# Optimization experiments

Hardware: AMD Instinct MI355X
Metric: run time of the kernel (lower is better)

## Reference

```python
import jax, jax.numpy as jnp
import numpy as np


def _conv(x, w):
    # SpykeTorch snn.Convolution: plain conv2d, no bias, no padding (VALID)
    return jax.lax.conv_general_dilated(
        x, w, window_strides=(1, 1), padding='VALID',
        dimension_numbers=('NCHW', 'OIHW', 'NCHW'))


def _pad2(x, p=2):
    # sf.pad(input, pad=(2,2,2,2), value=0): zero-pad last two (spatial) dims
    return jnp.pad(x, ((0, 0), (0, 0), (p, p), (p, p)))


def _fire(pot, thr):
    # sf.fire: thresholded[pot <= thr] = 0 ; spk = thresholded.sign()
    thresholded = jnp.where(pot > thr, pot, jnp.zeros((), pot.dtype))
    spk = (pot > thr).astype(pot.dtype)
    return spk, thresholded


def _pool(x, k, s):
    # sf.pooling: max_pool2d, floor mode (== VALID reduce_window)
    return jax.lax.reduce_window(
        x, -jnp.inf, jax.lax.max,
        window_dimensions=(1, 1, k, k),
        window_strides=(1, 1, s, s),
        padding='VALID')


def setup_inputs() -> dict:
    key = jax.random.key(0)
    kx, k1, k2, k3 = jax.random.split(key, 4)
    # (T, C, H, W): T timesteps act as batch in SpykeTorch
    x = jax.random.uniform(kx, (20, 6, 160, 160), dtype=jnp.float32)

    def xavier_normal(k, shape):
        fan_in = shape[1] * shape[2] * shape[3]
        fan_out = shape[0] * shape[2] * shape[3]
        std = float(np.sqrt(2.0 / (fan_in + fan_out)))
        return jax.random.normal(k, shape, dtype=jnp.float32) * std

    w1 = xavier_normal(k1, (30, 6, 4, 4))
    w2 = xavier_normal(k2, (250, 30, 3, 3))
    w3 = xavier_normal(k3, (200, 250, 3, 3))
    return {'x': x, 'w1': w1, 'w2': w2, 'w3': w3, 'layer_idx': 3}


def reference(x, w1, w2, w3, layer_idx):
    # Eval-mode forward path of deepSNN up to `layer_idx` (tensor-returning branches)
    CONV1_T, CONV2_T, CONV3_T = 1.0, 1.0, 25.0
    inp = _pad2(x.astype(jnp.float32))          # (T,6,164,164)
    pot = _conv(inp, w1)                        # (T,30,161,161)
    spk, pot = _fire(pot, CONV1_T)
    if layer_idx == 1:
        return spk, pot
    pot = _conv(_pad2(_pool(spk, 2, 2)), w2)    # (T,250,82,82)
    spk, pot = _fire(pot, CONV2_T)
    if layer_idx == 2:
        return spk, pot
    pot = _conv(_pad2(_pool(spk, 3, 3)), w3)    # (T,200,29,29)
    spk, pot = _fire(pot, CONV3_T)
    return spk, pot
```

## Files before the change

kernel.cpp:

```cpp
#include <hip/hip_runtime.h>
#include <hip/hip_bf16.h>
#include <hip/hip_fp16.h>


#define OUT_HALF 3364000
#define MASK_PLANE 128000
#define T_FLOATS 168200

typedef float f32x16 __attribute__((ext_vector_type(16)));
typedef short bf8s __attribute__((ext_vector_type(8)));
typedef float f32x4 __attribute__((ext_vector_type(4)));
typedef float v2f __attribute__((ext_vector_type(2)));
typedef f32x4 f32x4u __attribute__((aligned(4)));

static __device__ __forceinline__ unsigned int pkbf(float a, float b) {
    union { __hip_bfloat162 h; unsigned int u; } cv;
    cv.h = __float22bfloat162_rn(make_float2(a, b));
    return cv.u;
}
static __device__ __forceinline__ unsigned short bfbits(float a) {
    union { __hip_bfloat16 h; unsigned short u; } cv;
    cv.h = __float2bfloat16(a);
    return cv.u;
}
static __device__ __forceinline__ v2f up2(unsigned int u) {
    union { unsigned int u32; __half2 h2; } cv; cv.u32 = u;
    float2 f = __half22float2(cv.h2);
    v2f r; r.x = f.x; r.y = f.y;
    return r;
}
static __device__ __forceinline__ unsigned long long expand32(unsigned int v) {
    unsigned long long x = v;
    x = (x | (x << 16)) & 0x0000FFFF0000FFFFull;
    x = (x | (x << 8))  & 0x00FF00FF00FF00FFull;
    x = (x | (x << 4))  & 0x0F0F0F0F0F0F0F0Full;
    x = (x | (x << 2))  & 0x3333333333333333ull;
    x = (x | (x << 1))  & 0x5555555555555555ull;
    return x;
}

__global__ __launch_bounds__(256) void k_conv1m(const float* __restrict__ x,
                                                const float* __restrict__ w1,
                                                const float* __restrict__ w2,
                                                unsigned int* __restrict__ w2h,
                                                unsigned int* __restrict__ mask1,
                                                unsigned int* __restrict__ flags2) {
    int tid = threadIdx.x;
    if (blockIdx.x >= 2000) {
        int tb = blockIdx.x - 2000;
        if (tb == 0)
            for (int i = tid; i < 540; i += 256) flags2[i] = 0u;
        int idx = tb * 256 + tid;
        int ck = idx >> 7, pl = idx & 127;
        int oc0 = 2 * pl, oc1 = oc0 + 1;
        float a = (oc0 < 250) ? w2[oc0 * 270 + ck] : 0.f;
        float bb = (oc1 < 250) ? w2[oc1 * 270 + ck] : 0.f;
        union { __half2 h2; unsigned int u; } cv;
        cv.h2.x = __float2half(a);
        cv.h2.y = __float2half(bb);
        w2h[idx] = cv.u;
        return;
    }

    __shared__ unsigned short B_lds[6 * 64 * 8];

#pragma unroll
    for (int n = 0; n < 12; ++n) {
        int q = n * 256 + tid;
        int i = q & 7, ll = (q >> 3) & 63, ks = q >> 9;
        int oc = ll & 31;
        int kg = ks * 16 + ((ll >> 5) << 3) + i;
        float w = (oc < 30) ? w1[oc * 96 + kg] : 0.f;
        B_lds[q] = bfbits(w);
    }
    __syncthreads();

    int l = tid & 63, wv = tid >> 6;
    int b = blockIdx.x;
    int t = b / 100;
    int u = (b % 100) * 4 + wv;
    int pr = u / 5, jblk = u % 5;
    int m = l & 31, hi = l >> 5;
    int j = jblk * 32 + m;

    bf8s bq[6];
#pragma unroll
    for (int ks = 0; ks < 6; ++ks)
        bq[ks] = *(const bf8s*)&B_lds[(ks * 64 + l) * 8];

    f32x16 acc0 = (f32x16)(0.0f);
    f32x16 acc1 = (f32x16)(0.0f);
    int sr0 = 2 * pr + 2 * hi - 2;
    int sc0 = j - 2;
    bool fast = ((unsigned)sr0 <= 157u) && ((unsigned)sc0 <= 156u);

#pragma unroll
    for (int ks = 0; ks < 6; ++ks) {
        const float* xp = x + (t * 6 + ks) * 25600;
        f32x4 v0, v1, v2;
        if (fast) {
            const float* bp = xp + sr0 * 160 + sc0;
            v0 = *(const f32x4u*)(bp);
            v1 = *(const f32x4u*)(bp + 160);
            v2 = *(const f32x4u*)(bp + 320);
        } else {
            float tmp[3][4];
#pragma unroll
            for (int r = 0; r < 3; ++r)
#pragma unroll
                for (int e = 0; e < 4; ++e) {
                    int sr = sr0 + r, sc = sc0 + e;
                    tmp[r][e] = ((unsigned)sr < 160u && (unsigned)sc < 160u)
                                    ? xp[sr * 160 + sc] : 0.f;
                }
            v0.x = tmp[0][0]; v0.y = tmp[0][1]; v0.z = tmp[0][2]; v0.w = tmp[0][3];
            v1.x = tmp[1][0]; v1.y = tmp[1][1]; v1.z = tmp[1][2]; v1.w = tmp[1][3];
            v2.x = tmp[2][0]; v2.y = tmp[2][1]; v2.z = tmp[2][2]; v2.w = tmp[2][3];
        }
        union { bf8s s; unsigned int u4[4]; } a0, a1;
        a0.u4[0] = pkbf(v0.x, v0.y);
        a0.u4[1] = pkbf(v0.z, v0.w);
        a0.u4[2] = pkbf(v1.x, v1.y);
        a0.u4[3] = pkbf(v1.z, v1.w);
        a1.u4[0] = a0.u4[2];
        a1.u4[1] = a0.u4[3];
        a1.u4[2] = pkbf(v2.x, v2.y);
        a1.u4[3] = pkbf(v2.z, v2.w);
        acc0 = __builtin_amdgcn_mfma_f32_32x32x16_bf16(a0.s, bq[ks], acc0, 0, 0, 0);
        acc1 = __builtin_amdgcn_mfma_f32_32x32x16_bf16(a1.s, bq[ks], acc1, 0, 0, 0);
    }

    unsigned int mbase = (unsigned int)((t * 80 + pr) * 80 + jblk * 16);
#pragma unroll
    for (int a = 0; a < 8; ++a) {
        bool s = acc0[2 * a] > 1.f || acc0[2 * a + 1] > 1.f ||
                 acc1[2 * a] > 1.f || acc1[2 * a + 1] > 1.f;
        unsigned long long bal = __ballot(s);
        if (l < 6) {
            int h = l >> 1;
            unsigned int word = (l & 1) ? (unsigned int)(bal >> 32)
                                        : (unsigned int)bal;
            int pc = (a & 1) + ((a >> 1) << 2) + ((l & 1) << 1);
            mask1[h * MASK_PLANE + mbase + pc] = (word >> (10 * h)) & 0x3FFu;
        }
    }
}

__global__ __launch_bounds__(256) void k_conv2(const unsigned int* __restrict__ mask1,
                                               const unsigned int* __restrict__ w2h,
                                               unsigned long long* __restrict__ pool2m,
                                               unsigned int* __restrict__ flags2) {
    __shared__ unsigned int m_lds[5 * 84];

    int b = blockIdx.x;
    int ninth = b % 9;  b /= 9;
    int ph = b % 27;
    int t = b / 27;
    int tid = threadIdx.x;
    int l = tid & 63, wv = tid >> 6;
    int h = wv & 1, grp = wv >> 1;
    int r0 = 3 * ph - 2;
    int pwA = ninth * 3;

    for (int idx = tid; idx < 420; idx += 256) {
        int r = idx / 84, col = idx % 84;
        int gr = r0 + r, gc = col - 2;
        unsigned int v = 0;
        if ((unsigned)gr < 80u && (unsigned)gc < 80u) {
            int i2 = (t * 80 + gr) * 80 + gc;
            v = mask1[i2] | (mask1[MASK_PLANE + i2] << 10) |
                (mask1[2 * MASK_PLANE + i2] << 20);
        }
        m_lds[idx] = v;
    }
    __syncthreads();

    const unsigned int* wb = w2h + h * 64 + l;
    unsigned long long* prow = pool2m + ((t * 27 + ph) * 27) * 4 + 2 * h;
    v2f z2 = (v2f)(0.f);

    if (grp == 0) {
        int c0A = 3 * pwA, c0B = c0A + 3;
        unsigned int qA[25], qB[25];
#pragma unroll
        for (int dr = 0; dr < 5; ++dr)
#pragma unroll
            for (int ds = 0; ds < 5; ++ds) {
                qA[dr * 5 + ds] = m_lds[dr * 84 + c0A + ds];
                qB[dr * 5 + ds] = m_lds[dr * 84 + c0B + ds];
            }

        v2f accA[3][3], accB[3][3];
#pragma unroll
        for (int i = 0; i < 3; ++i)
#pragma unroll
            for (int j = 0; j < 3; ++j) { accA[i][j] = z2; accB[i][j] = z2; }

#pragma unroll
        for (int dr = 0; dr < 5; ++dr) {
#pragma unroll
            for (int ds = 0; ds < 5; ++ds) {
                unsigned int mA = qA[dr * 5 + ds];
                unsigned int mB = qB[dr * 5 + ds];
                while (mA | mB) {
                    bool hA = mA != 0, hB = mB != 0;
                    int cA = __builtin_ctz(mA | 0x40000000u);
                    int cB = __builtin_ctz(mB | 0x40000000u);
                    mA &= mA - 1;
                    mB &= mB - 1;
                    const unsigned int* pA = wb + cA * 1152;
                    const unsigned int* pB = wb + cB * 1152;
                    unsigned int uA[3][3], uB[3][3];
#pragma unroll
                    for (int i = 0; i < 3; ++i) {
                        if (dr - i < 0 || dr - i > 2) continue;
#pragma unroll
                        for (int j = 0; j < 3; ++j) {
                            if (ds - j < 0 || ds - j > 2) continue;
                            int off = ((dr - i) * 3 + (ds - j)) * 128;
                            uA[i][j] = pA[off];
                            uB[i][j] = pB[off];
                        }
                    }
#pragma unroll
                    for (int i = 0; i < 3; ++i) {
                        if (dr - i < 0 || dr - i > 2) continue;
#pragma unroll
                        for (int j = 0; j < 3; ++j) {
                            if (ds - j < 0 || ds - j > 2) continue;
                            accA[i][j] += hA ? up2(uA[i][j]) : z2;
                            accB[i][j] += hB ? up2(uB[i][j]) : z2;
                        }
                    }
                }
            }
        }

        bool sA0 = false, sA1 = false, sB0 = false, sB1 = false;
#pragma unroll
        for (int i = 0; i < 3; ++i)
#pragma unroll
            for (int j = 0; j < 3; ++j) {
                sA0 = sA0 || (accA[i][j].x > 1.f);
                sA1 = sA1 || (accA[i][j].y > 1.f);
                sB0 = sB0 || (accB[i][j].x > 1.f);
                sB1 = sB1 || (accB[i][j].y > 1.f);
            }
        unsigned long long bA0 = __ballot(sA0), bA1 = __ballot(sA1);
        unsigned long long bB0 = __ballot(sB0), bB1 = __ballot(sB1);
        unsigned long long wA0 = expand32((unsigned int)bA0) |
                                 (expand32((unsigned int)bA1) << 1);
        unsigned long long wA1 = expand32((unsigned int)(bA0 >> 32)) |
                                 (expand32((unsigned int)(bA1 >> 32)) << 1);
        unsigned long long wB0 = expand32((unsigned int)bB0) |
                                 (expand32((unsigned int)bB1) << 1);
        unsigned long long wB1 = expand32((unsigned int)(bB0 >> 32)) |
                                 (expand32((unsigned int)(bB1 >> 32)) << 1);
        if (l == 0) {
            prow[pwA * 4]           = wA0;
            prow[pwA * 4 + 1]       = wA1;
            prow[(pwA + 1) * 4]     = wB0;
            prow[(pwA + 1) * 4 + 1] = wB1;
        }
        if ((wA0 | wA1 | wB0 | wB1) && l == 0)
            flags2[t * 27 + ph] = 1u;
    } else {
        int pw = pwA + 2;
        int c0 = 3 * pw;
        unsigned int q[25];
#pragma unroll
        for (int dr = 0; dr < 5; ++dr)
#pragma unroll
            for (int ds = 0; ds < 5; ++ds)
                q[dr * 5 + ds] = m_lds[dr * 84 + c0 + ds];

        v2f acc[3][3];
#pragma unroll
        for (int i = 0; i < 3; ++i)
#pragma unroll
            for (int j = 0; j < 3; ++j) acc[i][j] = z2;

#pragma unroll
        for (int dr = 0; dr < 5; ++dr) {
#pragma unroll
            for (int ds = 0; ds < 5; ++ds) {
                unsigned int m = q[dr * 5 + ds];
                while (m) {
                    int c1 = __builtin_ctz(m); m &= m - 1;
                    bool has2 = (m != 0);
                    int c2 = c1;
                    if (has2) { c2 = __builtin_ctz(m); m &= m - 1; }
                    const unsigned int* p1 = wb + c1 * 1152;
                    const unsigned int* p2 = wb + c2 * 1152;
                    unsigned int u1[3][3], u2[3][3];
#pragma unroll
                    for (int i = 0; i < 3; ++i) {
                        if (dr - i < 0 || dr - i > 2) continue;
#pragma unroll
                        for (int j = 0; j < 3; ++j) {
                            if (ds - j < 0 || ds - j > 2) continue;
                            int off = ((dr - i) * 3 + (ds - j)) * 128;
                            u1[i][j] = p1[off];
                            u2[i][j] = p2[off];
                        }
                    }
#pragma unroll
                    for (int i = 0; i < 3; ++i) {
                        if (dr - i < 0 || dr - i > 2) continue;
#pragma unroll
                        for (int j = 0; j < 3; ++j) {
                            if (ds - j < 0 || ds - j > 2) continue;
                            acc[i][j] += up2(u1[i][j]);
                            acc[i][j] += has2 ? up2(u2[i][j]) : z2;
                        }
                    }
                }
            }
        }

        bool s0 = false, s1 = false;
#pragma unroll
        for (int i = 0; i < 3; ++i)
#pragma unroll
            for (int j = 0; j < 3; ++j) {
                s0 = s0 || (acc[i][j].x > 1.f);
                s1 = s1 || (acc[i][j].y > 1.f);
            }
        unsigned long long b0 = __ballot(s0), b1 = __ballot(s1);
        unsigned long long w0 = expand32((unsigned int)b0) |
                                (expand32((unsigned int)b1) << 1);
        unsigned long long w1 = expand32((unsigned int)(b0 >> 32)) |
                                (expand32((unsigned int)(b1 >> 32)) << 1);
        if (l == 0) {
            prow[pw * 4]     = w0;
            prow[pw * 4 + 1] = w1;
        }
        if ((w0 | w1) && l == 0) flags2[t * 27 + ph] = 1u;
    }
}

__global__ __launch_bounds__(320) void k_conv3(const unsigned long long* __restrict__ pool2m,
                                               const float* __restrict__ w3,
                                               float* __restrict__ out,
                                               const unsigned int* __restrict__ flags2) {
    __shared__ float w_lds[25 * 9 * 40];
    __shared__ float in_lds[25 * 4 * 34];

    int b = blockIdx.x;
    int rb = b % 15;  b /= 15;
    int ocg = b % 5;  b /= 5;
    int t = b;
    int oc0 = ocg * 40;
    int r0 = 2 * rb;
    int tid = threadIdx.x;
    int ocl = tid % 40, ct = tid / 40;

    {
        unsigned int fT = 0;
        const unsigned int* fp = flags2 + t * 27;
#pragma unroll
        for (int r = 0; r < 27; ++r) fT |= fp[r];
        if (fT == 0) {
            float4 z; z.x = 0.f; z.y = 0.f; z.z = 0.f; z.w = 0.f;
            float4* o0 = (float4*)(out + (size_t)t * T_FLOATS);
            float4* o1 = (float4*)(out + OUT_HALF + (size_t)t * T_FLOATS);
            int s = ocg * 15 + rb;
            int lo = s * 561;
            int hi = lo + 561; if (hi > 42050) hi = 42050;
            for (int i = lo + tid; i < hi; i += 320) {
                o0[i] = z;
                o1[i] = z;
            }
            return;
        }
    }

    {
        unsigned int f = 0;
        int rlo = r0 - 2; if (rlo < 0) rlo = 0;
        int rhi = r0 + 1; if (rhi > 26) rhi = 26;
        for (int r = rlo; r <= rhi; ++r) f |= flags2[t * 27 + r];
        if (f == 0) {
            int nrows = (r0 + 1 < 29) ? 2 : 1;
            int stride = 29 * nrows;
            int cnt = 40 * stride;
            for (int idx = tid; idx < cnt; idx += 320) {
                int o = idx / stride, rem = idx % stride;
                size_t base = (size_t)((t * 200 + oc0 + o) * 29 + r0) * 29 + rem;
                out[base] = 0.f;
                out[OUT_HALF + base] = 0.f;
            }
            return;
        }
    }

    float acc[2][4];
#pragma unroll
    for (int i = 0; i < 2; ++i)
#pragma unroll
        for (int j = 0; j < 4; ++j) acc[i][j] = 0.f;

    for (int chn = 0; chn < 10; ++chn) {
        int cc0 = chn * 25;
        for (int idx = tid; idx < 25 * 9 * 40; idx += 320) {
            int o = idx % 40, ck = idx / 40;
            int ckg = cc0 * 9 + ck;
            w_lds[idx] = w3[(size_t)(oc0 + o) * 2250 + ckg];
        }
        for (int idx = tid; idx < 25 * 4 * 34; idx += 320) {
            int col = idx % 34;
            int rem = idx / 34;
            int r = rem & 3, cl = rem >> 2;
            int gr = r0 + r - 2, gc = col - 2;
            float v = 0.f;
            if ((unsigned)gr < 27u && (unsigned)gc < 27u) {
                int c = cc0 + cl;
                unsigned long long wbits =
                    pool2m[((t * 27 + gr) * 27 + gc) * 4 + (c >> 6)];
                v = (float)((wbits >> (c & 63)) & 1ull);
            }
            in_lds[idx] = v;
        }
        __syncthreads();

        for (int cl = 0; cl < 25; ++cl) {
            float in[4][6];
#pragma unroll
            for (int r = 0; r < 4; ++r)
#pragma unroll
                for (int j = 0; j < 6; ++j)
                    in[r][j] = in_lds[(cl * 4 + r) * 34 + ct * 4 + j];
            const float* wp = &w_lds[cl * 360 + ocl];
#pragma unroll
            for (int k = 0; k < 9; ++k) {
                float w = wp[k * 40];
                int kh = k / 3, kw = k % 3;
#pragma unroll
                for (int i = 0; i < 2; ++i)
#pragma unroll
                    for (int j = 0; j < 4; ++j)
                        acc[i][j] += in[i + kh][j + kw] * w;
            }
        }
        __syncthreads();
    }

    {
        int oc = oc0 + ocl;
#pragma unroll
        for (int i = 0; i < 2; ++i) {
            int r = r0 + i;
            if (r < 29) {
#pragma unroll
                for (int j = 0; j < 4; ++j) {
                    int col = ct * 4 + j;
                    if (col < 29) {
                        float pot = acc[i][j];
                        bool s = pot > 25.f;
                        size_t base = ((size_t)((t * 200 + oc) * 29 + r)) * 29 + col;
                        out[base] = s ? 1.f : 0.f;
                        out[OUT_HALF + base] = s ? pot : 0.f;
                    }
                }
            }
        }
    }
}

extern "C" void kernel_launch(void* const* d_in, const int* in_sizes, int n_in,
                              void* d_out, int out_size, void* d_ws, size_t ws_size,
                              hipStream_t stream) {
    const float* x  = (const float*)d_in[0];
    const float* w1 = (const float*)d_in[1];
    const float* w2 = (const float*)d_in[2];
    const float* w3 = (const float*)d_in[3];
    float* out = (float*)d_out;

    unsigned int* mask1 = (unsigned int*)d_ws;
    unsigned long long* pool2m = (unsigned long long*)((char*)d_ws + 1536000);
    unsigned int* w2h = (unsigned int*)((char*)d_ws + 2002560);
    unsigned int* flags2 = (unsigned int*)((char*)d_ws + 2277376);

    k_conv1m<<<2135, 256, 0, stream>>>(x, w1, w2, w2h, mask1, flags2);
    k_conv2<<<20 * 27 * 9, 256, 0, stream>>>(mask1, w2h, pool2m, flags2);
    k_conv3<<<20 * 5 * 15, 320, 0, stream>>>(pool2m, w3, out, flags2);
}
```

Baseline: 124.9 us.

## Replace sparse scalar conv2 with bf16 MFMA im2col over binary spike mask

Conv2 previously walked the set bits of the spike mask and accumulated fp16 weights in scalar registers. It now builds a dense bf16 im2col tile of 0/1 spikes in LDS and runs 32x32x16 bf16 MFMA with weights held in registers. The weight prepack changes to a bf16 fragment layout, and the grid becomes one 512-thread block per (t, pooled row) instead of nine per row. This removes divergent, data-dependent gather loops at the cost of doing dense work on sparse inputs, with bf16 rounding of the weights.

```diff
diff --git a/kernel.cpp b/kernel.cpp
--- a/kernel.cpp
+++ b/kernel.cpp
@@ -1,6 +1,5 @@
 #include <hip/hip_runtime.h>
 #include <hip/hip_bf16.h>
-#include <hip/hip_fp16.h>
 
 
 #define OUT_HALF 3364000
@@ -10,7 +9,6 @@
 typedef float f32x16 __attribute__((ext_vector_type(16)));
 typedef short bf8s __attribute__((ext_vector_type(8)));
 typedef float f32x4 __attribute__((ext_vector_type(4)));
-typedef float v2f __attribute__((ext_vector_type(2)));
 typedef f32x4 f32x4u __attribute__((aligned(4)));
 
 static __device__ __forceinline__ unsigned int pkbf(float a, float b) {
@@ -23,26 +21,11 @@
     cv.h = __float2bfloat16(a);
     return cv.u;
 }
-static __device__ __forceinline__ v2f up2(unsigned int u) {
-    union { unsigned int u32; __half2 h2; } cv; cv.u32 = u;
-    float2 f = __half22float2(cv.h2);
-    v2f r; r.x = f.x; r.y = f.y;
-    return r;
-}
-static __device__ __forceinline__ unsigned long long expand32(unsigned int v) {
-    unsigned long long x = v;
-    x = (x | (x << 16)) & 0x0000FFFF0000FFFFull;
-    x = (x | (x << 8))  & 0x00FF00FF00FF00FFull;
-    x = (x | (x << 4))  & 0x0F0F0F0F0F0F0F0Full;
-    x = (x | (x << 2))  & 0x3333333333333333ull;
-    x = (x | (x << 1))  & 0x5555555555555555ull;
-    return x;
-}
 
 __global__ __launch_bounds__(256) void k_conv1m(const float* __restrict__ x,
                                                 const float* __restrict__ w1,
                                                 const float* __restrict__ w2,
-                                                unsigned int* __restrict__ w2h,
+                                                unsigned short* __restrict__ w2b,
                                                 unsigned int* __restrict__ mask1,
                                                 unsigned int* __restrict__ flags2) {
     int tid = threadIdx.x;
@@ -51,14 +34,15 @@
         if (tb == 0)
             for (int i = tid; i < 540; i += 256) flags2[i] = 0u;
         int idx = tb * 256 + tid;
-        int ck = idx >> 7, pl = idx & 127;
-        int oc0 = 2 * pl, oc1 = oc0 + 1;
-        float a = (oc0 < 250) ? w2[oc0 * 270 + ck] : 0.f;
-        float bb = (oc1 < 250) ? w2[oc1 * 270 + ck] : 0.f;
-        union { __half2 h2; unsigned int u; } cv;
-        cv.h2.x = __float2half(a);
-        cv.h2.y = __float2half(bb);
-        w2h[idx] = cv.u;
+        int i8 = idx & 7;
+        int ll = (idx >> 3) & 63;
+        int gi = idx >> 9;
+        int ocg = (gi * 1928) >> 15;
+        int ks = gi - ocg * 17;
+        int oc = ocg * 32 + (ll & 31);
+        int k = ks * 16 + ((ll >> 5) << 3) + i8;
+        float w = (oc < 250 && k < 270) ? w2[oc * 270 + k] : 0.f;
+        w2b[idx] = bfbits(w);
         return;
     }
 
@@ -146,24 +130,30 @@
     }
 }
 
-__global__ __launch_bounds__(256) void k_conv2(const unsigned int* __restrict__ mask1,
-                                               const unsigned int* __restrict__ w2h,
-                                               unsigned long long* __restrict__ pool2m,
+__global__ __launch_bounds__(512) void k_conv2(const unsigned int* __restrict__ mask1,
+                                               const unsigned short* __restrict__ w2b,
+                                               unsigned int* __restrict__ pool2m32,
                                                unsigned int* __restrict__ flags2) {
     __shared__ unsigned int m_lds[5 * 84];
+    __shared__ unsigned short A_lds[96 * 280];
 
     int b = blockIdx.x;
-    int ninth = b % 9;  b /= 9;
-    int ph = b % 27;
-    int t = b / 27;
+    int ph = b % 27, t = b / 27;
     int tid = threadIdx.x;
     int l = tid & 63, wv = tid >> 6;
-    int h = wv & 1, grp = wv >> 1;
+    int m = l & 31, hi = l >> 5;
     int r0 = 3 * ph - 2;
-    int pwA = ninth * 3;
-
-    for (int idx = tid; idx < 420; idx += 256) {
-        int r = idx / 84, col = idx % 84;
+
+    bf8s bfr[17];
+    {
+        const unsigned short* wbp = w2b + (wv * 17 * 64 + l) * 8;
+#pragma unroll
+        for (int ks = 0; ks < 17; ++ks)
+            bfr[ks] = *(const bf8s*)(wbp + ks * 512);
+    }
+
+    if (tid < 420) {
+        int r = tid / 84, col = tid % 84;
         int gr = r0 + r, gc = col - 2;
         unsigned int v = 0;
         if ((unsigned)gr < 80u && (unsigned)gc < 80u) {
@@ -171,172 +161,91 @@
             v = mask1[i2] | (mask1[MASK_PLANE + i2] << 10) |
                 (mask1[2 * MASK_PLANE + i2] << 20);
         }
-        m_lds[idx] = v;
+        m_lds[tid] = v;
     }
     __syncthreads();
 
-    const unsigned int* wb = w2h + h * 64 + l;
-    unsigned long long* prow = pool2m + ((t * 27 + ph) * 27) * 4 + 2 * h;
-    v2f z2 = (v2f)(0.f);
-
-    if (grp == 0) {
-        int c0A = 3 * pwA, c0B = c0A + 3;
-        unsigned int qA[25], qB[25];
-#pragma unroll
-        for (int dr = 0; dr < 5; ++dr)
-#pragma unroll
-            for (int ds = 0; ds < 5; ++ds) {
-                qA[dr * 5 + ds] = m_lds[dr * 84 + c0A + ds];
-                qB[dr * 5 + ds] = m_lds[dr * 84 + c0B + ds];
-            }
-
-        v2f accA[3][3], accB[3][3];
-#pragma unroll
-        for (int i = 0; i < 3; ++i)
-#pragma unroll
-            for (int j = 0; j < 3; ++j) { accA[i][j] = z2; accB[i][j] = z2; }
-
-#pragma unroll
-        for (int dr = 0; dr < 5; ++dr) {
-#pragma unroll
-            for (int ds = 0; ds < 5; ++ds) {
-                unsigned int mA = qA[dr * 5 + ds];
-                unsigned int mB = qB[dr * 5 + ds];
-                while (mA | mB) {
-                    bool hA = mA != 0, hB = mB != 0;
-                    int cA = __builtin_ctz(mA | 0x40000000u);
-                    int cB = __builtin_ctz(mB | 0x40000000u);
-                    mA &= mA - 1;
-                    mB &= mB - 1;
-                    const unsigned int* pA = wb + cA * 1152;
-                    const unsigned int* pB = wb + cB * 1152;
-                    unsigned int uA[3][3], uB[3][3];
-#pragma unroll
-                    for (int i = 0; i < 3; ++i) {
-                        if (dr - i < 0 || dr - i > 2) continue;
-#pragma unroll
-                        for (int j = 0; j < 3; ++j) {
-                            if (ds - j < 0 || ds - j > 2) continue;
-                            int off = ((dr - i) * 3 + (ds - j)) * 128;
-                            uA[i][j] = pA[off];
-                            uB[i][j] = pB[off];
-                        }
-                    }
-#pragma unroll
-                    for (int i = 0; i < 3; ++i) {
-                        if (dr - i < 0 || dr - i > 2) continue;
-#pragma unroll
-                        for (int j = 0; j < 3; ++j) {
-                            if (ds - j < 0 || ds - j > 2) continue;
-                            accA[i][j] += hA ? up2(uA[i][j]) : z2;
-                            accB[i][j] += hB ? up2(uB[i][j]) : z2;
-                        }
-                    }
+    unsigned int rowor[3] = {0u, 0u, 0u};
+
+#pragma unroll
+    for (int rho = 0; rho < 3; ++rho) {
+        if (rho > 0) __syncthreads();
+
+        if (tid < 164) {
+            int s = tid >> 1;
+            unsigned int w[9];
+#pragma unroll
+            for (int tp = 0; tp < 9; ++tp)
+                w[tp] = m_lds[(rho + tp / 3) * 84 + s + (tp % 3)];
+            if ((tid & 1) == 0) {
+                unsigned int* dst = (unsigned int*)&A_lds[s * 280];
+#pragma unroll
+                for (int kp = 0; kp < 68; ++kp) {
+                    const int k0 = 2 * kp, k1 = k0 + 1;
+                    unsigned int v = 0;
+                    { const int c = k0 / 9, tp = k0 % 9;
+                      v |= ((w[tp] >> c) & 1u) ? 0x3F80u : 0u; }
+                    { const int c = k1 / 9, tp = k1 % 9;
+                      v |= ((w[tp] >> c) & 1u) ? 0x3F800000u : 0u; }
+                    dst[kp] = v;
                 }
-            }
-        }
-
-        bool sA0 = false, sA1 = false, sB0 = false, sB1 = false;
-#pragma unroll
-        for (int i = 0; i < 3; ++i)
-#pragma unroll
-            for (int j = 0; j < 3; ++j) {
-                sA0 = sA0 || (accA[i][j].x > 1.f);
-                sA1 = sA1 || (accA[i][j].y > 1.f);
-                sB0 = sB0 || (accB[i][j].x > 1.f);
-                sB1 = sB1 || (accB[i][j].y > 1.f);
-            }
-        unsigned long long bA0 = __ballot(sA0), bA1 = __ballot(sA1);
-        unsigned long long bB0 = __ballot(sB0), bB1 = __ballot(sB1);
-        unsigned long long wA0 = expand32((unsigned int)bA0) |
-                                 (expand32((unsigned int)bA1) << 1);
-        unsigned long long wA1 = expand32((unsigned int)(bA0 >> 32)) |
-                                 (expand32((unsigned int)(bA1 >> 32)) << 1);
-        unsigned long long wB0 = expand32((unsigned int)bB0) |
-                                 (expand32((unsigned int)bB1) << 1);
-        unsigned long long wB1 = expand32((unsigned int)(bB0 >> 32)) |
-                                 (expand32((unsigned int)(bB1 >> 32)) << 1);
-        if (l == 0) {
-            prow[pwA * 4]           = wA0;
-            prow[pwA * 4 + 1]       = wA1;
-            prow[(pwA + 1) * 4]     = wB0;
-            prow[(pwA + 1) * 4 + 1] = wB1;
-        }
-        if ((wA0 | wA1 | wB0 | wB1) && l == 0)
-            flags2[t * 27 + ph] = 1u;
-    } else {
-        int pw = pwA + 2;
-        int c0 = 3 * pw;
-        unsigned int q[25];
-#pragma unroll
-        for (int dr = 0; dr < 5; ++dr)
-#pragma unroll
-            for (int ds = 0; ds < 5; ++ds)
-                q[dr * 5 + ds] = m_lds[dr * 84 + c0 + ds];
-
-        v2f acc[3][3];
-#pragma unroll
-        for (int i = 0; i < 3; ++i)
-#pragma unroll
-            for (int j = 0; j < 3; ++j) acc[i][j] = z2;
-
-#pragma unroll
-        for (int dr = 0; dr < 5; ++dr) {
-#pragma unroll
-            for (int ds = 0; ds < 5; ++ds) {
-                unsigned int m = q[dr * 5 + ds];
-                while (m) {
-                    int c1 = __builtin_ctz(m); m &= m - 1;
-                    bool has2 = (m != 0);
-                    int c2 = c1;
-                    if (has2) { c2 = __builtin_ctz(m); m &= m - 1; }
-                    const unsigned int* p1 = wb + c1 * 1152;
-                    const unsigned int* p2 = wb + c2 * 1152;
-                    unsigned int u1[3][3], u2[3][3];
-#pragma unroll
-                    for (int i = 0; i < 3; ++i) {
-                        if (dr - i < 0 || dr - i > 2) continue;
-#pragma unroll
-                        for (int j = 0; j < 3; ++j) {
-                            if (ds - j < 0 || ds - j > 2) continue;
-                            int off = ((dr - i) * 3 + (ds - j)) * 128;
-                            u1[i][j] = p1[off];
-                            u2[i][j] = p2[off];
-                        }
-                    }
-#pragma unroll
-                    for (int i = 0; i < 3; ++i) {
-                        if (dr - i < 0 || dr - i > 2) continue;
-#pragma unroll
-                        for (int j = 0; j < 3; ++j) {
-                            if (ds - j < 0 || ds - j > 2) continue;
-                            acc[i][j] += up2(u1[i][j]);
-                            acc[i][j] += has2 ? up2(u2[i][j]) : z2;
-                        }
-                    }
+            } else {
+                unsigned int* dst = (unsigned int*)&A_lds[s * 280 + 136];
+#pragma unroll
+                for (int kp = 0; kp < 68; ++kp) {
+                    const int k0 = 136 + 2 * kp, k1 = k0 + 1;
+                    unsigned int v = 0;
+                    if (k0 < 270) { const int c = k0 / 9, tp = k0 % 9;
+                                    v |= ((w[tp] >> c) & 1u) ? 0x3F80u : 0u; }
+                    if (k1 < 270) { const int c = k1 / 9, tp = k1 % 9;
+                                    v |= ((w[tp] >> c) & 1u) ? 0x3F800000u : 0u; }
+                    dst[kp] = v;
                 }
             }
         }
-
-        bool s0 = false, s1 = false;
-#pragma unroll
-        for (int i = 0; i < 3; ++i)
-#pragma unroll
-            for (int j = 0; j < 3; ++j) {
-                s0 = s0 || (acc[i][j].x > 1.f);
-                s1 = s1 || (acc[i][j].y > 1.f);
-            }
-        unsigned long long b0 = __ballot(s0), b1 = __ballot(s1);
-        unsigned long long w0 = expand32((unsigned int)b0) |
-                                (expand32((unsigned int)b1) << 1);
-        unsigned long long w1 = expand32((unsigned int)(b0 >> 32)) |
-                                (expand32((unsigned int)(b1 >> 32)) << 1);
-        if (l == 0) {
-            prow[pw * 4]     = w0;
-            prow[pw * 4 + 1] = w1;
-        }
-        if ((w0 | w1) && l == 0) flags2[t * 27 + ph] = 1u;
-    }
+        __syncthreads();
+
+#pragma unroll
+        for (int ct = 0; ct < 3; ++ct) {
+            f32x16 acc = (f32x16)(0.0f);
+            const unsigned short* ap = &A_lds[(ct * 32 + m) * 280 + hi * 8];
+#pragma unroll
+            for (int ks = 0; ks < 17; ++ks) {
+                bf8s af = *(const bf8s*)(ap + ks * 16);
+                acc = __builtin_amdgcn_mfma_f32_32x32x16_bf16(af, bfr[ks], acc, 0, 0, 0);
+            }
+            unsigned int cm = 0;
+#pragma unroll
+            for (int a = 0; a < 16; ++a) {
+                int col = (a & 3) + 8 * (a >> 2) + 4 * hi;
+                cm |= (acc[a] > 1.f) ? (1u << col) : 0u;
+            }
+            cm |= __shfl_xor(cm, 32);
+            rowor[ct] |= cm;
+        }
+    }
+
+    unsigned long long lo = (unsigned long long)rowor[0] |
+                            ((unsigned long long)rowor[1] << 32);
+    unsigned int mid = (rowor[1] >> 31) | (rowor[2] << 1);
+    unsigned int pooled = 0;
+#pragma unroll
+    for (int pc = 0; pc < 21; ++pc)
+        pooled |= ((lo >> (3 * pc)) & 7ull) ? (1u << pc) : 0u;
+#pragma unroll
+    for (int pc = 21; pc < 27; ++pc)
+        pooled |= ((mid >> (3 * (pc - 21))) & 7u) ? (1u << pc) : 0u;
+
+    unsigned int base = (unsigned int)((t * 27 + ph) * 27) * 8;
+    unsigned int orAll = 0;
+#pragma unroll
+    for (int pc = 0; pc < 27; ++pc) {
+        unsigned long long bal = __ballot((pooled >> pc) & 1u);
+        unsigned int wrd = (unsigned int)bal;
+        if (l == pc) pool2m32[base + pc * 8 + wv] = wrd;
+        orAll |= wrd;
+    }
+    if (l == 0 && orAll) flags2[t * 27 + ph] = 1u;
 }
 
 __global__ __launch_bounds__(320) void k_conv3(const unsigned long long* __restrict__ pool2m,
@@ -478,10 +387,10 @@
 
     unsigned int* mask1 = (unsigned int*)d_ws;
     unsigned long long* pool2m = (unsigned long long*)((char*)d_ws + 1536000);
-    unsigned int* w2h = (unsigned int*)((char*)d_ws + 2002560);
+    unsigned short* w2b = (unsigned short*)((char*)d_ws + 2002560);
     unsigned int* flags2 = (unsigned int*)((char*)d_ws + 2277376);
 
-    k_conv1m<<<2135, 256, 0, stream>>>(x, w1, w2, w2h, mask1, flags2);
-    k_conv2<<<20 * 27 * 9, 256, 0, stream>>>(mask1, w2h, pool2m, flags2);
+    k_conv1m<<<2272, 256, 0, stream>>>(x, w1, w2, w2b, mask1, flags2);
+    k_conv2<<<20 * 27, 512, 0, stream>>>(mask1, w2b, (unsigned int*)pool2m, flags2);
     k_conv3<<<20 * 5 * 15, 320, 0, stream>>>(pool2m, w3, out, flags2);
 }
```

After: 134.5 us. 1.08x slower.
